# Optimization experiments

Hardware: AMD Instinct MI355X
Metric: run time of the kernel (lower is better)

## Reference

```python
import jax, jax.numpy as jnp
import numpy as np

L, H, C, V, B, T, Q = 6, 8, 512, 32000, 2, 4096, 256
N = C // H
LN_EPS = 1e-5
GN_EPS = 1e-5 * 64  # matches nn.GroupNorm(n_head, C, eps=1e-05*64)


def _shift(x):
    # ZeroPad2d((0,0,1,-1)): x[t] -> x[t-1], zero at t=0
    return jnp.concatenate([jnp.zeros_like(x[:, :1]), x[:, :-1]], axis=1)


def _layernorm(x, w):
    mu = x.mean(-1, keepdims=True)
    var = jnp.var(x, axis=-1, keepdims=True)
    return (x - mu) * jax.lax.rsqrt(var + LN_EPS) * w


def _time_mix(x, maa_k, maa_v, maa_r, maa_g, tdecay, tfaaaa, Wr, Wk, Wv, Wg, Wo, gn_w, gn_b):
    Bsz, Tlen, Cd = x.shape
    xx = _shift(x) - x
    xk = x + xx * maa_k
    xv = x + xx * maa_v
    xr = x + xx * maa_r
    xg = x + xx * maa_g
    r = (xr @ Wr.T).reshape(Bsz, Tlen, H, N).transpose(0, 2, 1, 3)   # B H T N
    k = (xk @ Wk.T).reshape(Bsz, Tlen, H, N).transpose(0, 2, 3, 1)   # B H N T
    v = (xv @ Wv.T).reshape(Bsz, Tlen, H, N).transpose(0, 2, 1, 3)   # B H T N
    g = jax.nn.silu(xg @ Wg.T)
    wdec = jnp.exp(-jnp.exp(tdecay))            # [H], per-head decay in (0,1)
    u = tfaaaa                                  # [H], 'first token' bonus
    ws = (wdec ** Q)[None, :, None, None]       # state decay across a chunk
    jj = jnp.arange(Q)
    wkv = (wdec[:, None] ** (Q - 1 - jj))[None, :, None, :]  # [1,H,1,Q]
    wb = (wdec[:, None] ** jj)[None, :, :, None]              # [1,H,Q,1]
    d = jj[:, None] - jj[None, :]                              # i - j
    # intra-chunk decay matrix: W[i,j] = u (i==j), wdec^(i-j-1) (i>j), 0 (i<j)
    Wmat = jnp.where(d > 0, wdec[:, None, None] ** jnp.maximum(d - 1, 0), 0.0)
    Wmat = (Wmat + u[:, None, None] * jnp.eye(Q, dtype=x.dtype))[None]  # [1,H,Q,Q]
    nc = Tlen // Q
    rc = r.reshape(Bsz, H, nc, Q, N).transpose(2, 0, 1, 3, 4)  # [nc,B,H,Q,N]
    kc = k.reshape(Bsz, H, N, nc, Q).transpose(3, 0, 1, 2, 4)  # [nc,B,H,N,Q]
    vc = v.reshape(Bsz, H, nc, Q, N).transpose(2, 0, 1, 3, 4)  # [nc,B,H,Q,N]

    def step(state, inp):
        rr, kk, vv = inp
        y = ((rr @ kk) * Wmat) @ vv + (rr @ state) * wb
        new_state = ws * state + (kk * wkv) @ vv
        return new_state, y

    state0 = jnp.zeros((Bsz, H, N, N), dtype=x.dtype)
    _, yc = jax.lax.scan(step, state0, (rc, kc, vc))
    y = yc.transpose(1, 2, 0, 3, 4).reshape(Bsz, H, Tlen, N).transpose(0, 2, 1, 3)  # B T H N
    # GroupNorm(n_head groups) == per (b,t,h) normalization over head dim N
    mu = y.mean(-1, keepdims=True)
    var = jnp.var(y, axis=-1, keepdims=True)
    y = (y - mu) * jax.lax.rsqrt(var + GN_EPS)
    y = y.reshape(Bsz, Tlen, Cd) * gn_w + gn_b
    return (y * g) @ Wo.T


def _channel_mix(x, cmaa_k, cmaa_r, Wck, Wcv, Wcr):
    xx = _shift(x) - x
    xk = x + xx * cmaa_k
    xr = x + xx * cmaa_r
    h = jnp.square(jax.nn.relu(xk @ Wck.T))
    h = h @ Wcv.T
    return jax.nn.sigmoid(xr @ Wcr.T) * h


def _forward(idx, wte, wpe, ln1_w, ln2_w, lnf_w, maa_k, maa_v, maa_r, maa_g, tdecay, tfaaaa,
             Wr, Wk, Wv, Wg, Wo, gn_w, gn_b, cmaa_k, cmaa_r, Wck, Wcv, Wcr):
    t = idx.shape[1]
    x = wte[idx] + wpe[:t]
    for l in range(L):
        x = x + _time_mix(_layernorm(x, ln1_w[l]), maa_k[l], maa_v[l], maa_r[l], maa_g[l],
                          tdecay[l], tfaaaa[l], Wr[l], Wk[l], Wv[l], Wg[l], Wo[l], gn_w[l], gn_b[l])
        x = x + _channel_mix(_layernorm(x, ln2_w[l]), cmaa_k[l], cmaa_r[l], Wck[l], Wcv[l], Wcr[l])
    x = _layernorm(x, lnf_w)
    logits = x[:, -1:, :] @ wte.T  # targets=None path: only last position
    return logits


def setup_inputs() -> dict:
    key = jax.random.key(0)
    ks = jax.random.split(key, 12)
    idx = jax.random.randint(ks[0], (B, T), 0, V)
    # structured per-layer init tensors (exact formulas from __init__)
    ddd = np.arange(C, dtype=np.float32) / C
    hh = np.arange(H, dtype=np.float32) / (H - 1)
    maa_k = np.zeros((L, C), np.float32); maa_v = np.zeros((L, C), np.float32)
    maa_r = np.zeros((L, C), np.float32); maa_g = np.zeros((L, C), np.float32)
    tdecay = np.zeros((L, H), np.float32); tfaaaa = np.zeros((L, H), np.float32)
    cmaa_k = np.zeros((L, C), np.float32); cmaa_r = np.zeros((L, C), np.float32)
    for l in range(L):
        r0 = l / max(L - 1, 1)
        r1 = 1.0 - l / L
        maa_k[l] = 1.0 - ddd ** r1
        maa_v[l] = 1.0 - (ddd ** r1 + 0.3 * r0)
        maa_r[l] = 1.0 - ddd ** (0.5 * r1)
        maa_g[l] = 1.0 - ddd ** (0.5 * r1)
        tdecay[l] = -6.0 + 5.0 * hh ** (0.7 + 1.3 * r0)
        tfaaaa[l] = r0 * (1.0 - hh)
        cmaa_k[l] = 1.0 - ddd ** r1
        cmaa_r[l] = 1.0 - ddd ** r1
    s = 0.02
    return {
        'idx': idx,
        'wte': jax.random.normal(ks[1], (V, C), jnp.float32) * s,
        'wpe': jax.random.normal(ks[2], (T, C), jnp.float32) * s,
        'ln1_w': jnp.ones((L, C), jnp.float32),
        'ln2_w': jnp.ones((L, C), jnp.float32),
        'lnf_w': jnp.ones((C,), jnp.float32),
        'maa_k': jnp.asarray(maa_k), 'maa_v': jnp.asarray(maa_v),
        'maa_r': jnp.asarray(maa_r), 'maa_g': jnp.asarray(maa_g),
        'tdecay': jnp.asarray(tdecay), 'tfaaaa': jnp.asarray(tfaaaa),
        'Wr': jax.random.normal(ks[3], (L, C, C), jnp.float32) * s,
        'Wk': jax.random.normal(ks[4], (L, C, C), jnp.float32) * s,
        'Wv': jax.random.normal(ks[5], (L, C, C), jnp.float32) * s,
        'Wg': jax.random.normal(ks[6], (L, C, C), jnp.float32) * s,
        'Wo': jax.random.normal(ks[7], (L, C, C), jnp.float32) * (s / np.sqrt(2 * L)),
        'gn_w': jnp.ones((L, C), jnp.float32),
        'gn_b': jnp.zeros((L, C), jnp.float32),
        'cmaa_k': jnp.asarray(cmaa_k), 'cmaa_r': jnp.asarray(cmaa_r),
        'Wck': jax.random.normal(ks[8], (L, 3 * C, C), jnp.float32) * s,
        'Wcv': jax.random.normal(ks[9], (L, C, 3 * C), jnp.float32) * s,
        'Wcr': jax.random.normal(ks[10], (L, C, C), jnp.float32) * s,
    }


def reference(idx, wte, wpe, ln1_w, ln2_w, lnf_w, maa_k, maa_v, maa_r, maa_g, tdecay, tfaaaa,
              Wr, Wk, Wv, Wg, Wo, gn_w, gn_b, cmaa_k, cmaa_r, Wck, Wcv, Wcr):
    return _forward(idx, wte, wpe, ln1_w, ln2_w, lnf_w, maa_k, maa_v, maa_r, maa_g, tdecay,
                    tfaaaa, Wr, Wk, Wv, Wg, Wo, gn_w, gn_b, cmaa_k, cmaa_r, Wck, Wcv, Wcr)
```

## Files before the change

kernel.cpp:

```cpp
#include <hip/hip_runtime.h>

#define L_ 6
#define H_ 8
#define C_ 512
#define V_ 32000
#define B_ 2
#define T_ 4096
#define Q_ 256
#define N_ 64
#define NC_ 16
#define M_ 8192

typedef unsigned short u16;
typedef __attribute__((ext_vector_type(8))) short bf16x8;
typedef __attribute__((ext_vector_type(4))) float f32x4;

__device__ __forceinline__ float bf2f(u16 u){
  return __uint_as_float(((unsigned int)u) << 16);
}
__device__ __forceinline__ u16 f2bf(float f){
  unsigned int x = __float_as_uint(f);
  return (u16)((x + 0x7fffu + ((x >> 16) & 1u)) >> 16);
}

__device__ __forceinline__ void gl_lds16(const u16* g, u16* l){
  __builtin_amdgcn_global_load_lds((const __attribute__((address_space(1))) void*)g,
                                   (__attribute__((address_space(3))) void*)l, 16, 0, 0);
}

__global__ __launch_bounds__(256) void detect_kernel(const void* __restrict__ probe,
                                                     int* __restrict__ flag){
  __shared__ int cnt;
  if (threadIdx.x == 0) cnt = 0;
  __syncthreads();
  const u16* p = (const u16*)probe;
  int c = 0;
  for (int i = threadIdx.x; i < 2048; i += 256){
    int e = (p[i] >> 7) & 0xFF;
    if (e >= 128) c++;
  }
  atomicAdd(&cnt, c);
  __syncthreads();
  if (threadIdx.x == 0) *flag = (cnt > 32) ? 1 : 0;
}

struct CvtTab { const void* s[23]; int off8[24]; };

__global__ __launch_bounds__(256) void convert_all(CvtTab t, u16* __restrict__ pool,
                                                   const int* __restrict__ flag){
  const bool f32 = (*flag != 0);
  const int total = t.off8[23];
  uint4* dp = (uint4*)pool;
  const int stride = gridDim.x * 256;
  for (int j = blockIdx.x*256 + threadIdx.x; j < total; j += stride){
    int i = 0;
    #pragma unroll
    for (int k = 1; k < 23; k++) if (j >= t.off8[k]) i = k;
    const int loc = j - t.off8[i];
    uint4 r;
    if (f32){
      const float4* sf = (const float4*)t.s[i];
      float4 a = sf[2*loc], b = sf[2*loc+1];
      r.x = (unsigned)f2bf(a.x) | ((unsigned)f2bf(a.y) << 16);
      r.y = (unsigned)f2bf(a.z) | ((unsigned)f2bf(a.w) << 16);
      r.z = (unsigned)f2bf(b.x) | ((unsigned)f2bf(b.y) << 16);
      r.w = (unsigned)f2bf(b.z) | ((unsigned)f2bf(b.w) << 16);
    } else {
      r = ((const uint4*)t.s[i])[loc];
    }
    dp[j] = r;
  }
}

__global__ __launch_bounds__(256) void embed_kernel(const int* __restrict__ idx,
    const u16* __restrict__ wte, const u16* __restrict__ wpe, float* __restrict__ x){
  int row = blockIdx.x;
  int t = row & (T_-1);
  int tok = idx[row];
  const u16* we = wte + (size_t)tok * C_;
  const u16* wp = wpe + (size_t)t * C_;
  float* xo = x + (size_t)row * C_;
  int c = threadIdx.x;
  xo[c]     = bf2f(we[c])     + bf2f(wp[c]);
  xo[c+256] = bf2f(we[c+256]) + bf2f(wp[c+256]);
}

__global__ __launch_bounds__(256) void ln_tmix_kernel(const float* __restrict__ x,
    const u16* __restrict__ w,
    const u16* __restrict__ mk, const u16* __restrict__ mv,
    const u16* __restrict__ mr, const u16* __restrict__ mg,
    u16* __restrict__ xk, u16* __restrict__ xv, u16* __restrict__ xr, u16* __restrict__ xg){
  int row = blockIdx.x; int t = row & (T_-1);
  size_t off = (size_t)row*C_;
  const float* cur = x + off;
  int c = threadIdx.x;
  float v0 = cur[c], v1 = cur[c+256];
  float p0 = 0.f, p1 = 0.f;
  if (t){ p0 = cur[c - C_]; p1 = cur[c+256 - C_]; }
  float s = v0+v1, ss = v0*v0+v1*v1;
  float sp = p0+p1, ssp = p0*p0+p1*p1;
  int lane = c & 63, wid = c >> 6;
  #pragma unroll
  for (int o=32;o>0;o>>=1){
    s  += __shfl_down(s,o,64);  ss  += __shfl_down(ss,o,64);
    sp += __shfl_down(sp,o,64); ssp += __shfl_down(ssp,o,64);
  }
  __shared__ float r1[4], r2[4], r3[4], r4[4];
  if (lane==0){ r1[wid]=s; r2[wid]=ss; r3[wid]=sp; r4[wid]=ssp; }
  __syncthreads();
  if (c==0){
    float a =r1[0]+r1[1]+r1[2]+r1[3], bq=r2[0]+r2[1]+r2[2]+r2[3];
    float ap=r3[0]+r3[1]+r3[2]+r3[3], bp=r4[0]+r4[1]+r4[2]+r4[3];
    float mu  = a *(1.f/C_); float var  = bq*(1.f/C_) - mu*mu;
    float mup = ap*(1.f/C_); float varp = bp*(1.f/C_) - mup*mup;
    r1[0]=mu;  r2[0]=rsqrtf(fmaxf(var ,0.f)+1e-5f);
    r3[0]=mup; r4[0]=rsqrtf(fmaxf(varp,0.f)+1e-5f);
  }
  __syncthreads();
  float mu=r1[0], inv=r2[0], mup=r3[0], invp=r4[0];
  #pragma unroll
  for (int p=0;p<2;p++){
    int cc = c + p*256;
    float wc = bf2f(w[cc]);
    float xc = ((p?v1:v0)-mu)*inv*wc;
    float xp = t ? ((p?p1:p0)-mup)*invp*wc : 0.f;
    float xx = xp - xc;
    xk[off+cc] = f2bf(xc + xx*bf2f(mk[cc]));
    xv[off+cc] = f2bf(xc + xx*bf2f(mv[cc]));
    xr[off+cc] = f2bf(xc + xx*bf2f(mr[cc]));
    xg[off+cc] = f2bf(xc + xx*bf2f(mg[cc]));
  }
}

__global__ __launch_bounds__(256) void ln_cmix_kernel(const float* __restrict__ x,
    const u16* __restrict__ w,
    const u16* __restrict__ mk, const u16* __restrict__ mr,
    u16* __restrict__ xk, u16* __restrict__ xr){
  int row = blockIdx.x; int t = row & (T_-1);
  size_t off = (size_t)row*C_;
  const float* cur = x + off;
  int c = threadIdx.x;
  float v0 = cur[c], v1 = cur[c+256];
  float p0 = 0.f, p1 = 0.f;
  if (t){ p0 = cur[c - C_]; p1 = cur[c+256 - C_]; }
  float s = v0+v1, ss = v0*v0+v1*v1;
  float sp = p0+p1, ssp = p0*p0+p1*p1;
  int lane = c & 63, wid = c >> 6;
  #pragma unroll
  for (int o=32;o>0;o>>=1){
    s  += __shfl_down(s,o,64);  ss  += __shfl_down(ss,o,64);
    sp += __shfl_down(sp,o,64); ssp += __shfl_down(ssp,o,64);
  }
  __shared__ float r1[4], r2[4], r3[4], r4[4];
  if (lane==0){ r1[wid]=s; r2[wid]=ss; r3[wid]=sp; r4[wid]=ssp; }
  __syncthreads();
  if (c==0){
    float a =r1[0]+r1[1]+r1[2]+r1[3], bq=r2[0]+r2[1]+r2[2]+r2[3];
    float ap=r3[0]+r3[1]+r3[2]+r3[3], bp=r4[0]+r4[1]+r4[2]+r4[3];
    float mu  = a *(1.f/C_); float var  = bq*(1.f/C_) - mu*mu;
    float mup = ap*(1.f/C_); float varp = bp*(1.f/C_) - mup*mup;
    r1[0]=mu;  r2[0]=rsqrtf(fmaxf(var ,0.f)+1e-5f);
    r3[0]=mup; r4[0]=rsqrtf(fmaxf(varp,0.f)+1e-5f);
  }
  __syncthreads();
  float mu=r1[0], inv=r2[0], mup=r3[0], invp=r4[0];
  #pragma unroll
  for (int p=0;p<2;p++){
    int cc = c + p*256;
    float wc = bf2f(w[cc]);
    float xc = ((p?v1:v0)-mu)*inv*wc;
    float xp = t ? ((p?p1:p0)-mup)*invp*wc : 0.f;
    float xx = xp - xc;
    xk[off+cc] = f2bf(xc + xx*bf2f(mk[cc]));
    xr[off+cc] = f2bf(xc + xx*bf2f(mr[cc]));
  }
}

__global__ __launch_bounds__(256) void lnf_last(const float* __restrict__ x,
    const u16* __restrict__ w, float* __restrict__ xf){
  int b = blockIdx.x;
  const float* xr = x + ((size_t)b*T_ + (T_-1))*C_;
  int c = threadIdx.x;
  float v0 = xr[c], v1 = xr[c+256];
  float s = v0+v1, ss = v0*v0+v1*v1;
  int lane = c & 63, wid = c >> 6;
  #pragma unroll
  for (int o=32;o>0;o>>=1){ s += __shfl_down(s,o,64); ss += __shfl_down(ss,o,64); }
  __shared__ float r1[4], r2[4];
  if (lane==0){ r1[wid]=s; r2[wid]=ss; }
  __syncthreads();
  if (c==0){
    float a=r1[0]+r1[1]+r1[2]+r1[3], bq=r2[0]+r2[1]+r2[2]+r2[3];
    float mu = a*(1.f/C_);
    float var = bq*(1.f/C_) - mu*mu;
    r1[0]=mu; r2[0]=rsqrtf(fmaxf(var,0.f)+1e-5f);
  }
  __syncthreads();
  float mu=r1[0], inv=r2[0];
  xf[b*C_+c]     = (v0-mu)*inv*bf2f(w[c]);
  xf[b*C_+c+256] = (v1-mu)*inv*bf2f(w[c+256]);
}

#define ACT_F32 0
#define ACT_RELU2_BF16 1
#define ACT_ADD_F32 2
#define ACT_BF16 3
#define ACT_CMIX 4
#define ACT_KT 5
#define ACT_VT 6

template<int ACT>
__device__ __forceinline__ void gemm_mfma_body(const u16* __restrict__ X, const u16* __restrict__ W,
    float* __restrict__ Yf, u16* __restrict__ Yb, const float* __restrict__ Aux,
    u16* __restrict__ Yt, const u16* __restrict__ td,
    int Ndim, int Kdim, int bm, int bn){
  __shared__ __align__(16) u16 Al[128*64];
  __shared__ __align__(16) u16 Bl[64*64];
  const int tid = threadIdx.x;
  const int wv = tid >> 6, ln = tid & 63;
  const int m16 = ln & 15, q = ln >> 4;

  f32x4 acc[2][4];
  #pragma unroll
  for (int i=0;i<2;i++)
    #pragma unroll
    for (int j=0;j<4;j++) acc[i][j] = f32x4{0.f,0.f,0.f,0.f};

  const int r0 = wv*8 + (ln >> 3);
  const int c0 = (ln & 7)*8;
  const u16* ga = X + (size_t)(bm + r0)*Kdim + c0;
  const u16* gb = W + (size_t)(bn + r0)*Kdim + c0;
  u16* la = Al + r0*64 + c0;
  u16* lb = Bl + r0*64 + c0;

  for (int k0=0; k0<Kdim; k0+=64){
    #pragma unroll
    for (int s=0;s<4;s++)
      gl_lds16(ga + (size_t)(s*32)*Kdim + k0, la + s*2048);
    #pragma unroll
    for (int s=0;s<2;s++)
      gl_lds16(gb + (size_t)(s*32)*Kdim + k0, lb + s*2048);
    __syncthreads();
    #pragma unroll
    for (int kh=0; kh<2; kh++){
      bf16x8 af[2], bfr[4];
      #pragma unroll
      for (int i=0;i<2;i++) af[i]  = *(const bf16x8*)(Al + (wv*32 + i*16 + m16)*64 + kh*32 + q*8);
      #pragma unroll
      for (int j=0;j<4;j++) bfr[j] = *(const bf16x8*)(Bl + (j*16 + m16)*64 + kh*32 + q*8);
      #pragma unroll
      for (int i=0;i<2;i++)
        #pragma unroll
        for (int j=0;j<4;j++)
          acc[i][j] = __builtin_amdgcn_mfma_f32_16x16x32_bf16(af[i], bfr[j], acc[i][j], 0, 0, 0);
    }
    __syncthreads();
  }

  if (ACT==ACT_KT || ACT==ACT_VT){
    float wdec_s = 0.f;
    if (ACT==ACT_KT) wdec_s = expf(-expf(bf2f(td[bn>>6])));
    #pragma unroll
    for (int i=0;i<2;i++){
      int row = bm + wv*32 + i*16 + q*4;
      int bb = row >> 12;
      int tt = row & (T_-1);
      int tloc = row & (Q_-1);
      float wsc[4];
      if (ACT==ACT_KT){
        #pragma unroll
        for (int r=0;r<4;r++) wsc[r] = powf(wdec_s, (float)(Q_-1-tloc-r));
      }
      #pragma unroll
      for (int j=0;j<4;j++){
        int col = bn + j*16 + m16;
        int hh = col >> 6, n = col & 63;
        union { ushort4 v; u16 e[4]; } pk;
        #pragma unroll
        for (int r=0;r<4;r++){
          float v = acc[i][j][r];
          if (ACT==ACT_KT){
            Yb[(size_t)(row+r)*Ndim + col] = f2bf(v);
            pk.e[r] = f2bf(v * wsc[r]);
          } else {
            pk.e[r] = f2bf(v);
          }
        }
        *(ushort4*)(Yt + ((size_t)((bb*8+hh)*64 + n))*T_ + tt) = pk.v;
      }
    }
    return;
  }
  #pragma unroll
  for (int i=0;i<2;i++){
    int row = bm + wv*32 + i*16 + q*4;
    #pragma unroll
    for (int j=0;j<4;j++){
      int col = bn + j*16 + m16;
      #pragma unroll
      for (int r=0;r<4;r++){
        size_t off = (size_t)(row + r)*Ndim + col;
        float v = acc[i][j][r];
        if (ACT==ACT_F32) Yf[off] = v;
        else if (ACT==ACT_RELU2_BF16){ float rr = v>0.f ? v : 0.f; Yb[off] = f2bf(rr*rr); }
        else if (ACT==ACT_BF16) Yb[off] = f2bf(v);
        else if (ACT==ACT_CMIX){ float rr = Aux[off]; Yf[off] += v/(1.f+expf(-rr)); }
        else Yf[off] += v;
      }
    }
  }
}

template<int ACT>
__global__ __launch_bounds__(256,4) void gemm_mfma(const u16* __restrict__ X, const u16* __restrict__ W,
    float* __restrict__ Yf, u16* __restrict__ Yb, int Ndim, int Kdim){
  gemm_mfma_body<ACT>(X, W, Yf, Yb, nullptr, nullptr, nullptr, Ndim, Kdim,
                      blockIdx.x*128, blockIdx.y*64);
}

__global__ __launch_bounds__(256,4) void gemm4_mfma(const u16* __restrict__ Abase,
    const u16* __restrict__ W0, const u16* __restrict__ W1,
    const u16* __restrict__ W2, const u16* __restrict__ W3,
    u16* __restrict__ Rb, u16* __restrict__ Kb, u16* __restrict__ Kt,
    u16* __restrict__ Vt, u16* __restrict__ Gb, const u16* __restrict__ td){
  const size_t MC = (size_t)M_*C_;
  const int bm = blockIdx.x*128, bn = blockIdx.y*64;
  switch (blockIdx.z){
    case 0:  gemm_mfma_body<ACT_BF16>(Abase + 2*MC, W0, nullptr, Rb, nullptr, nullptr, nullptr,
                                      C_, C_, bm, bn); break;
    case 1:  gemm_mfma_body<ACT_KT>(Abase, W1, nullptr, Kb, nullptr, Kt, td,
                                    C_, C_, bm, bn); break;
    case 2:  gemm_mfma_body<ACT_VT>(Abase + 1*MC, W2, nullptr, nullptr, nullptr, Vt, nullptr,
                                    C_, C_, bm, bn); break;
    default: gemm_mfma_body<ACT_BF16>(Abase + 3*MC, W3, nullptr, Gb, nullptr, nullptr, nullptr,
                                      C_, C_, bm, bn); break;
  }
}

__global__ __launch_bounds__(256,4) void gemm_ck_cr(const u16* __restrict__ MK, const u16* __restrict__ Wck,
    u16* __restrict__ H1, const u16* __restrict__ MV, const u16* __restrict__ Wcr,
    float* __restrict__ RR){
  if (blockIdx.y < 24)
    gemm_mfma_body<ACT_RELU2_BF16>(MK, Wck, nullptr, H1, nullptr, nullptr, nullptr, 3*C_, C_,
                                   blockIdx.x*128, blockIdx.y*64);
  else
    gemm_mfma_body<ACT_F32>(MV, Wcr, RR, nullptr, nullptr, nullptr, nullptr, C_, C_,
                            blockIdx.x*128, (blockIdx.y-24)*64);
}

__global__ __launch_bounds__(256,4) void gemm_cmix(const u16* __restrict__ H1, const u16* __restrict__ Wcv,
    float* __restrict__ X, const float* __restrict__ RR){
  gemm_mfma_body<ACT_CMIX>(H1, Wcv, X, nullptr, RR, nullptr, nullptr, C_, 3*C_,
                           blockIdx.x*128, blockIdx.y*64);
}

__global__ __launch_bounds__(256) void wkv_intra_mfma(const u16* __restrict__ Rb,
    const u16* __restrict__ Kb, const u16* __restrict__ Vt,
    const u16* __restrict__ td, const u16* __restrict__ tf, float* __restrict__ y){
  __shared__ float wpow[Q_];
  __shared__ __align__(16) u16 P[4][16][72];
  const int c = blockIdx.x >> 2, ip = blockIdx.x & 3;
  const int bh = blockIdx.y, b = bh >> 3, h = bh & 7;
  const int tid = threadIdx.x, wv = tid >> 6, ln = tid & 63;
  const int m16 = ln & 15, q = ln >> 4;
  const float wdec = expf(-expf(bf2f(td[h])));
  const float uu = bf2f(tf[h]);
  wpow[tid] = powf(wdec, (float)tid);
  __syncthreads();
  const size_t base = ((size_t)b*T_ + (size_t)c*Q_)*C_ + h*N_;
  const int iw0 = ip*64 + wv*16;
  const u16* rrow = Rb + base + (size_t)(iw0 + m16)*C_;
  bf16x8 af0 = *(const bf16x8*)(rrow + q*8);
  bf16x8 af1 = *(const bf16x8*)(rrow + 32 + q*8);
  f32x4 acc[4];
  #pragma unroll
  for (int nt=0;nt<4;++nt) acc[nt] = f32x4{0.f,0.f,0.f,0.f};
  const int irow = iw0 + q*4;
  const u16* vtb = Vt + (size_t)(bh*N_)*T_ + (size_t)c*Q_;
  for (int jt=0; jt<=ip; ++jt){
    f32x4 s[4];
    #pragma unroll
    for (int j2=0;j2<4;++j2) s[j2] = f32x4{0.f,0.f,0.f,0.f};
    #pragma unroll
    for (int j2=0;j2<4;++j2){
      const u16* kr = Kb + base + (size_t)(jt*64 + j2*16 + m16)*C_;
      bf16x8 b0 = *(const bf16x8*)(kr + q*8);
      bf16x8 b1 = *(const bf16x8*)(kr + 32 + q*8);
      s[j2] = __builtin_amdgcn_mfma_f32_16x16x32_bf16(af0, b0, s[j2], 0,0,0);
      s[j2] = __builtin_amdgcn_mfma_f32_16x16x32_bf16(af1, b1, s[j2], 0,0,0);
    }
    #pragma unroll
    for (int j2=0;j2<4;++j2){
      int jc = jt*64 + j2*16 + m16;
      #pragma unroll
      for (int r=0;r<4;++r){
        int ic = irow + r;
        float w = (jc < ic) ? wpow[ic-jc-1] : ((jc==ic) ? uu : 0.f);
        P[wv][q*4+r][j2*16+m16] = f2bf(s[j2][r]*w);
      }
    }
    __asm__ volatile("s_waitcnt lgkmcnt(0)" ::: "memory");
    #pragma unroll
    for (int kp=0;kp<2;++kp){
      bf16x8 ap = *(const bf16x8*)&P[wv][m16][kp*32 + q*8];
      #pragma unroll
      for (int nt=0;nt<4;++nt){
        bf16x8 bv = *(const bf16x8*)(vtb + (size_t)(nt*16 + m16)*T_ + jt*64 + kp*32 + q*8);
        acc[nt] = __builtin_amdgcn_mfma_f32_16x16x32_bf16(ap, bv, acc[nt], 0,0,0);
      }
    }
  }
  #pragma unroll
  for (int nt=0;nt<4;++nt)
    #pragma unroll
    for (int r=0;r<4;++r)
      y[base + (size_t)(irow + r)*C_ + nt*16 + m16] = acc[nt][r];
}

__global__ __launch_bounds__(256) void wkv_state_mfma(const u16* __restrict__ Kt,
    const u16* __restrict__ Vt, float* __restrict__ S){
  const int c = blockIdx.x, bh = blockIdx.y;
  const int tid = threadIdx.x, wv = tid >> 6, ln = tid & 63;
  const int m16 = ln & 15, q = ln >> 4;
  const u16* ka = Kt + (size_t)(bh*N_ + wv*16 + m16)*T_ + c*Q_;
  const u16* vb = Vt + (size_t)(bh*N_ + m16)*T_ + c*Q_;
  f32x4 acc[4];
  #pragma unroll
  for (int nt=0;nt<4;++nt) acc[nt] = f32x4{0.f,0.f,0.f,0.f};
  #pragma unroll
  for (int ks=0; ks<8; ++ks){
    bf16x8 af = *(const bf16x8*)(ka + ks*32 + q*8);
    #pragma unroll
    for (int nt=0;nt<4;++nt){
      bf16x8 bv = *(const bf16x8*)(vb + (size_t)(nt*16)*T_ + ks*32 + q*8);
      acc[nt] = __builtin_amdgcn_mfma_f32_16x16x32_bf16(af, bv, acc[nt], 0,0,0);
    }
  }
  float* Sp = S + ((size_t)bh*NC_ + c)*(N_*N_);
  #pragma unroll
  for (int nt=0;nt<4;++nt)
    #pragma unroll
    for (int r=0;r<4;++r)
      Sp[(wv*16 + q*4 + r)*N_ + nt*16 + m16] = acc[nt][r];
}

__global__ __launch_bounds__(256) void wkv_prefix(float* __restrict__ S, const u16* __restrict__ td){
  const int bh = blockIdx.x, h = bh&7;
  const float wdec = expf(-expf(bf2f(td[h])));
  const float wsd = powf(wdec, (float)Q_);
  float* Sp = S + (size_t)bh*NC_*N_*N_;
  for (int e=threadIdx.x; e<N_*N_; e+=256){
    float cur = 0.f;
    for (int cc=0;cc<NC_;++cc){
      float sc = Sp[(size_t)cc*N_*N_ + e];
      Sp[(size_t)cc*N_*N_ + e] = cur;
      cur = wsd*cur + sc;
    }
  }
}

__global__ __launch_bounds__(256) void wkv_inter_gn(const u16* __restrict__ Rb, const float* __restrict__ S,
    const u16* __restrict__ td, const float* __restrict__ y,
    const u16* __restrict__ gnw, const u16* __restrict__ gnb, const u16* __restrict__ g,
    u16* __restrict__ out){
  __shared__ float st[64][65];
  __shared__ float rs[64][68];
  __shared__ float wpow[Q_];
  const int c = blockIdx.x>>2, ip = blockIdx.x&3;
  const int bh = blockIdx.y, b = bh>>3, h = bh&7;
  const int tid = threadIdx.x, tx = tid&15, ty = tid>>4;
  const float wdec = expf(-expf(bf2f(td[h])));
  wpow[tid] = powf(wdec, (float)tid);
  const float* Sp = S + ((size_t)bh*NC_ + c)*(N_*N_);
  for (int e=tid;e<N_*N_;e+=256) st[e>>6][e&63] = Sp[e];
  const size_t base = ((size_t)b*T_ + (size_t)c*Q_)*C_ + h*N_;
  const int i0 = ip*64;
  {
    const int rr = tid >> 6, cc2 = tid & 63;
    for (int it=0;it<16;++it){ int i=it*4+rr; rs[i][cc2]=bf2f(Rb[base+(size_t)(i0+i)*C_+cc2]); }
  }
  __syncthreads();
  float acc[4][4] = {};
  for (int kk=0;kk<N_;++kk){
    float rv[4], sv[4];
    #pragma unroll
    for (int ii=0;ii<4;ii++) rv[ii]=rs[ty*4+ii][kk];
    #pragma unroll
    for (int nn=0;nn<4;nn++) sv[nn]=st[kk][tx*4+nn];
    #pragma unroll
    for (int ii=0;ii<4;ii++)
      #pragma unroll
      for (int nn=0;nn<4;nn++) acc[ii][nn]+=rv[ii]*sv[nn];
  }
  #pragma unroll
  for (int ii=0;ii<4;ii++){
    int il = i0+ty*4+ii;
    size_t roff = base + (size_t)il*C_;
    float w = wpow[il];
    float4 yv = *(const float4*)(y + roff + tx*4);
    float val[4] = {yv.x, yv.y, yv.z, yv.w};
    float s=0.f, ss=0.f;
    #pragma unroll
    for (int nn=0;nn<4;nn++){
      float v = val[nn] + w*acc[ii][nn];
      val[nn]=v; s+=v; ss+=v*v;
    }
    #pragma unroll
    for (int o=8;o>0;o>>=1){ s+=__shfl_xor(s,o,64); ss+=__shfl_xor(ss,o,64); }
    float mu = s*(1.f/N_);
    float var = ss*(1.f/N_) - mu*mu;
    float inv = rsqrtf(fmaxf(var,0.f) + 6.4e-4f);
    union { ushort4 v; u16 e[4]; } gv, ov;
    gv.v = *(const ushort4*)(g + roff + tx*4);
    #pragma unroll
    for (int nn=0;nn<4;nn++){
      int ci = h*N_ + tx*4 + nn;
      float gg = bf2f(gv.e[nn]);
      float sil = gg/(1.f+expf(-gg));
      ov.e[nn] = f2bf(((val[nn]-mu)*inv*bf2f(gnw[ci]) + bf2f(gnb[ci]))*sil);
    }
    *(ushort4*)(out + roff + tx*4) = ov.v;
  }
}

__global__ __launch_bounds__(256) void logits_kernel(const float* __restrict__ xf,
    const u16* __restrict__ wte, void* __restrict__ out, const int* __restrict__ flag){
  const int wid = threadIdx.x>>6, lane = threadIdx.x&63;
  const int gw = blockIdx.x*4 + wid;
  const int b = gw / V_, v = gw - b*V_;
  const u16* wrow = wte + (size_t)v*C_;
  const float* xr = xf + b*C_;
  union {uint4 q; u16 h[8];} uu;
  uu.q = *(const uint4*)(wrow + lane*8);
  float s = 0.f;
  #pragma unroll
  for (int j=0;j<8;j++) s += bf2f(uu.h[j])*xr[lane*8+j];
  #pragma unroll
  for (int o=32;o>0;o>>=1) s += __shfl_down(s,o,64);
  if (lane==0){
    size_t o = (size_t)b*V_ + v;
    if (*flag) ((float*)out)[o] = s;
    else       ((u16*)out)[o]   = f2bf(s);
  }
}

extern "C" void kernel_launch(void* const* d_in, const int* in_sizes, int n_in,
                              void* d_out, int out_size, void* d_ws, size_t ws_size,
                              hipStream_t stream){
  (void)out_size; (void)ws_size; (void)n_in;
  const int* idx  = (const int*)d_in[0];

  char* ws = (char*)d_ws;
  const size_t MC  = (size_t)M_*C_;
  size_t o = 0;
  int* flag = (int*)(ws + o);            o += 1024;
  float* X   = (float*)(ws + o);         o += MC*4;
  float* Y   = (float*)(ws + o);         o += MC*4;
  u16* MK = (u16*)(ws + o);              o += MC*2;
  u16* MV = (u16*)(ws + o);              o += MC*2;
  u16* MR = (u16*)(ws + o);              o += MC*2;
  u16* MG = (u16*)(ws + o);              o += MC*2;
  u16* Rb = (u16*)(ws + o);              o += MC*2;
  u16* Kb = (u16*)(ws + o);              o += MC*2;
  u16* Kt = (u16*)(ws + o);              o += MC*2;
  u16* Gb = (u16*)(ws + o);              o += MC*2;
  u16* Vt = (u16*)(ws + o);              o += MC*2;
  float* XF = (float*)(ws + o);          o += 65536;
  u16* pool = (u16*)(ws + o);
  u16* YGN = MK;
  float* S  = (float*)MR;
  u16* H1 = Rb;
  float* RR = (float*)MR;

  detect_kernel<<<1,256,0,stream>>>(d_in[12], flag);
  u16* cw[24];
  CvtTab tab;
  {
    size_t poff = 0;
    int acc8 = 0;
    tab.off8[0] = 0;
    for (int i=1;i<24;i++){
      cw[i] = pool + poff; poff += (size_t)in_sizes[i];
      tab.s[i-1] = d_in[i];
      acc8 += in_sizes[i] >> 3;
      tab.off8[i] = acc8;
    }
  }
  convert_all<<<2048,256,0,stream>>>(tab, pool, flag);
  const u16* wte  = cw[1];  const u16* wpe  = cw[2];
  const u16* ln1w = cw[3];  const u16* ln2w = cw[4];  const u16* lnfw = cw[5];
  const u16* maak = cw[6];  const u16* maav = cw[7];
  const u16* maar = cw[8];  const u16* maag = cw[9];
  const u16* tdec = cw[10]; const u16* tfir = cw[11];
  const u16* Wr   = cw[12]; const u16* Wk   = cw[13]; const u16* Wv   = cw[14];
  const u16* Wg   = cw[15]; const u16* Wo   = cw[16];
  const u16* gnw  = cw[17]; const u16* gnb  = cw[18];
  const u16* cmk  = cw[19]; const u16* cmr  = cw[20];
  const u16* Wck  = cw[21]; const u16* Wcv  = cw[22]; const u16* Wcr  = cw[23];

  embed_kernel<<<M_,256,0,stream>>>(idx,wte,wpe,X);
  dim3 gsq(M_/128, C_/64);
  dim3 g4 (M_/128, C_/64, 4);
  dim3 gckcr(M_/128, 32);
  for (int l=0;l<L_;++l){
    ln_tmix_kernel<<<M_,256,0,stream>>>(X, ln1w+l*C_, maak+l*C_, maav+l*C_, maar+l*C_,
                                        maag+l*C_, MK,MV,MR,MG);
    gemm4_mfma<<<g4,256,0,stream>>>(MK, Wr+(size_t)l*C_*C_, Wk+(size_t)l*C_*C_,
                                    Wv+(size_t)l*C_*C_, Wg+(size_t)l*C_*C_,
                                    Rb, Kb, Kt, Vt, Gb, tdec+l*H_);
    wkv_intra_mfma<<<dim3(NC_*4, B_*H_),256,0,stream>>>(Rb,Kb,Vt, tdec+l*H_, tfir+l*H_, Y);
    wkv_state_mfma<<<dim3(NC_, B_*H_),256,0,stream>>>(Kt, Vt, S);
    wkv_prefix<<<B_*H_,256,0,stream>>>(S, tdec+l*H_);
    wkv_inter_gn<<<dim3(NC_*4, B_*H_),256,0,stream>>>(Rb, S, tdec+l*H_, Y,
                                                      gnw+l*C_, gnb+l*C_, Gb, YGN);
    gemm_mfma<ACT_ADD_F32><<<gsq,256,0,stream>>>(YGN, Wo+(size_t)l*C_*C_, X, nullptr, C_, C_);
    ln_cmix_kernel<<<M_,256,0,stream>>>(X, ln2w+l*C_, cmk+l*C_, cmr+l*C_, MK, MV);
    gemm_ck_cr<<<gckcr,256,0,stream>>>(MK, Wck+(size_t)l*3*C_*C_, H1,
                                       MV, Wcr+(size_t)l*C_*C_, RR);
    gemm_cmix<<<gsq,256,0,stream>>>(H1, Wcv+(size_t)l*C_*3*C_, X, RR);
  }
  lnf_last<<<B_,256,0,stream>>>(X, lnfw, XF);
  logits_kernel<<<(B_*V_)/4,256,0,stream>>>(XF, wte, d_out, flag);
}
```

Measured before the change: 1.667 ms.

## Fuse WKV intra/inter kernels, stage transposed K/V stores, bf16 sigmoid gate, per-tensor convert

Merges the intra-chunk WKV kernel into the inter-chunk GroupNorm kernel so the fp32 Y intermediate lives in LDS instead of round-tripping through global memory. The K/V transposed outputs are first staged in shared memory and written with coalesced 16-byte stores. The channel-mix receptance sigmoid is now computed in the Wcr GEMM epilogue and stored as bf16, which halves that buffer and moves the exp out of the cmix GEMM. The convert kernel assigns blocks per tensor and unrolls its loops. Risks: precision loss from the bf16 gate, higher LDS use in the fused kernel lowering occupancy, and a changed Wcv layer offset (3*C_*C_ vs C_*3*C_, which is numerically equal).

Result: no change. 1.673 ms (+0.4%).

```diff
diff --git a/kernel.cpp b/kernel.cpp
--- a/kernel.cpp
+++ b/kernel.cpp
@@ -44,31 +44,55 @@
   if (threadIdx.x == 0) *flag = (cnt > 32) ? 1 : 0;
 }
 
-struct CvtTab { const void* s[23]; int off8[24]; };
+struct CvtTab { const void* s[23]; int off8[24]; int bstart[24]; };
 
 __global__ __launch_bounds__(256) void convert_all(CvtTab t, u16* __restrict__ pool,
                                                    const int* __restrict__ flag){
-  const bool f32 = (*flag != 0);
-  const int total = t.off8[23];
-  uint4* dp = (uint4*)pool;
-  const int stride = gridDim.x * 256;
-  for (int j = blockIdx.x*256 + threadIdx.x; j < total; j += stride){
-    int i = 0;
-    #pragma unroll
-    for (int k = 1; k < 23; k++) if (j >= t.off8[k]) i = k;
-    const int loc = j - t.off8[i];
-    uint4 r;
-    if (f32){
-      const float4* sf = (const float4*)t.s[i];
-      float4 a = sf[2*loc], b = sf[2*loc+1];
-      r.x = (unsigned)f2bf(a.x) | ((unsigned)f2bf(a.y) << 16);
-      r.y = (unsigned)f2bf(a.z) | ((unsigned)f2bf(a.w) << 16);
-      r.z = (unsigned)f2bf(b.x) | ((unsigned)f2bf(b.y) << 16);
-      r.w = (unsigned)f2bf(b.z) | ((unsigned)f2bf(b.w) << 16);
-    } else {
-      r = ((const uint4*)t.s[i])[loc];
-    }
-    dp[j] = r;
+  int i = 0;
+  #pragma unroll
+  for (int k = 1; k < 23; k++) if ((int)blockIdx.x >= t.bstart[k]) i = k;
+  const void* sp = t.s[0];
+  #pragma unroll
+  for (int k = 1; k < 23; k++) if (i == k) sp = t.s[k];
+  const int n8 = t.off8[i+1] - t.off8[i];
+  const int nb = t.bstart[i+1] - t.bstart[i];
+  const int lb = (int)blockIdx.x - t.bstart[i];
+  uint4* dp = (uint4*)pool + t.off8[i];
+  const int stride = nb * 256;
+  int j = lb*256 + (int)threadIdx.x;
+  if (*flag){
+    const float4* sf = (const float4*)sp;
+    for (; j + stride < n8; j += 2*stride){
+      float4 a0 = sf[2*j], a1 = sf[2*j+1];
+      int j2 = j + stride;
+      float4 b0 = sf[2*j2], b1 = sf[2*j2+1];
+      uint4 r0, r1;
+      r0.x = (unsigned)f2bf(a0.x) | ((unsigned)f2bf(a0.y) << 16);
+      r0.y = (unsigned)f2bf(a0.z) | ((unsigned)f2bf(a0.w) << 16);
+      r0.z = (unsigned)f2bf(a1.x) | ((unsigned)f2bf(a1.y) << 16);
+      r0.w = (unsigned)f2bf(a1.z) | ((unsigned)f2bf(a1.w) << 16);
+      r1.x = (unsigned)f2bf(b0.x) | ((unsigned)f2bf(b0.y) << 16);
+      r1.y = (unsigned)f2bf(b0.z) | ((unsigned)f2bf(b0.w) << 16);
+      r1.z = (unsigned)f2bf(b1.x) | ((unsigned)f2bf(b1.y) << 16);
+      r1.w = (unsigned)f2bf(b1.z) | ((unsigned)f2bf(b1.w) << 16);
+      dp[j] = r0; dp[j2] = r1;
+    }
+    for (; j < n8; j += stride){
+      float4 a0 = sf[2*j], a1 = sf[2*j+1];
+      uint4 r0;
+      r0.x = (unsigned)f2bf(a0.x) | ((unsigned)f2bf(a0.y) << 16);
+      r0.y = (unsigned)f2bf(a0.z) | ((unsigned)f2bf(a0.w) << 16);
+      r0.z = (unsigned)f2bf(a1.x) | ((unsigned)f2bf(a1.y) << 16);
+      r0.w = (unsigned)f2bf(a1.z) | ((unsigned)f2bf(a1.w) << 16);
+      dp[j] = r0;
+    }
+  } else {
+    const uint4* s4 = (const uint4*)sp;
+    for (; j + 3*stride < n8; j += 4*stride){
+      uint4 a = s4[j], b = s4[j+stride], c = s4[j+2*stride], d = s4[j+3*stride];
+      dp[j] = a; dp[j+stride] = b; dp[j+2*stride] = c; dp[j+3*stride] = d;
+    }
+    for (; j < n8; j += stride) dp[j] = s4[j];
   }
 }
 
@@ -208,14 +232,16 @@
 #define ACT_CMIX 4
 #define ACT_KT 5
 #define ACT_VT 6
+#define ACT_SIG_BF16 7
 
 template<int ACT>
 __device__ __forceinline__ void gemm_mfma_body(const u16* __restrict__ X, const u16* __restrict__ W,
-    float* __restrict__ Yf, u16* __restrict__ Yb, const float* __restrict__ Aux,
+    float* __restrict__ Yf, u16* __restrict__ Yb, const u16* __restrict__ AuxB,
     u16* __restrict__ Yt, const u16* __restrict__ td,
     int Ndim, int Kdim, int bm, int bn){
-  __shared__ __align__(16) u16 Al[128*64];
-  __shared__ __align__(16) u16 Bl[64*64];
+  __shared__ __align__(16) u16 SH[128*64 + 64*64];
+  u16* Al = SH;
+  u16* Bl = SH + 128*64;
   const int tid = threadIdx.x;
   const int wv = tid >> 6, ln = tid & 63;
   const int m16 = ln & 15, q = ln >> 4;
@@ -258,37 +284,38 @@
   }
 
   if (ACT==ACT_KT || ACT==ACT_VT){
-    float wdec_s = 0.f;
-    if (ACT==ACT_KT) wdec_s = expf(-expf(bf2f(td[bn>>6])));
+    u16* TT = SH;
+    const float wdec_s = (ACT==ACT_KT) ? expf(-expf(bf2f(td[(bn>>6)&7]))) : 0.f;
+    const int tchunk0 = bm & (Q_-1);
     #pragma unroll
     for (int i=0;i<2;i++){
-      int row = bm + wv*32 + i*16 + q*4;
-      int bb = row >> 12;
-      int tt = row & (T_-1);
-      int tloc = row & (Q_-1);
-      float wsc[4];
-      if (ACT==ACT_KT){
-        #pragma unroll
-        for (int r=0;r<4;r++) wsc[r] = powf(wdec_s, (float)(Q_-1-tloc-r));
-      }
+      const int tloc = wv*32 + i*16 + q*4;
       #pragma unroll
       for (int j=0;j<4;j++){
-        int col = bn + j*16 + m16;
-        int hh = col >> 6, n = col & 63;
+        const int n = j*16 + m16;
         union { ushort4 v; u16 e[4]; } pk;
         #pragma unroll
         for (int r=0;r<4;r++){
           float v = acc[i][j][r];
           if (ACT==ACT_KT){
-            Yb[(size_t)(row+r)*Ndim + col] = f2bf(v);
-            pk.e[r] = f2bf(v * wsc[r]);
+            Yb[(size_t)(bm + tloc + r)*Ndim + (bn + n)] = f2bf(v);
+            pk.e[r] = f2bf(v * powf(wdec_s, (float)(Q_-1 - (tchunk0 + tloc + r))));
           } else {
             pk.e[r] = f2bf(v);
           }
         }
-        *(ushort4*)(Yt + ((size_t)((bb*8+hh)*64 + n))*T_ + tt) = pk.v;
+        *(ushort4*)&TT[n*136 + tloc] = pk.v;
       }
     }
+    __syncthreads();
+    const int bb = bm >> 12, tt0 = bm & (T_-1);
+    const int hh = (bn >> 6) & 7;
+    const int nn2 = wv*16 + (ln>>2), seg = ln & 3;
+    const u16* srcp = TT + nn2*136 + seg*32;
+    u16* dstp = Yt + ((size_t)(((bb<<3)+hh)*64 + nn2))*T_ + tt0 + seg*32;
+    #pragma unroll
+    for (int k2=0;k2<4;k2++)
+      *(uint4*)(dstp + k2*8) = *(const uint4*)(srcp + k2*8);
     return;
   }
   #pragma unroll
@@ -304,7 +331,8 @@
         if (ACT==ACT_F32) Yf[off] = v;
         else if (ACT==ACT_RELU2_BF16){ float rr = v>0.f ? v : 0.f; Yb[off] = f2bf(rr*rr); }
         else if (ACT==ACT_BF16) Yb[off] = f2bf(v);
-        else if (ACT==ACT_CMIX){ float rr = Aux[off]; Yf[off] += v/(1.f+expf(-rr)); }
+        else if (ACT==ACT_SIG_BF16) Yb[off] = f2bf(1.f/(1.f+expf(-v)));
+        else if (ACT==ACT_CMIX){ Yf[off] += v * bf2f(AuxB[off]); }
         else Yf[off] += v;
       }
     }
@@ -339,82 +367,19 @@
 
 __global__ __launch_bounds__(256,4) void gemm_ck_cr(const u16* __restrict__ MK, const u16* __restrict__ Wck,
     u16* __restrict__ H1, const u16* __restrict__ MV, const u16* __restrict__ Wcr,
-    float* __restrict__ RR){
+    u16* __restrict__ RRb){
   if (blockIdx.y < 24)
     gemm_mfma_body<ACT_RELU2_BF16>(MK, Wck, nullptr, H1, nullptr, nullptr, nullptr, 3*C_, C_,
                                    blockIdx.x*128, blockIdx.y*64);
   else
-    gemm_mfma_body<ACT_F32>(MV, Wcr, RR, nullptr, nullptr, nullptr, nullptr, C_, C_,
-                            blockIdx.x*128, (blockIdx.y-24)*64);
+    gemm_mfma_body<ACT_SIG_BF16>(MV, Wcr, nullptr, RRb, nullptr, nullptr, nullptr, C_, C_,
+                                 blockIdx.x*128, (blockIdx.y-24)*64);
 }
 
 __global__ __launch_bounds__(256,4) void gemm_cmix(const u16* __restrict__ H1, const u16* __restrict__ Wcv,
-    float* __restrict__ X, const float* __restrict__ RR){
-  gemm_mfma_body<ACT_CMIX>(H1, Wcv, X, nullptr, RR, nullptr, nullptr, C_, 3*C_,
+    float* __restrict__ X, const u16* __restrict__ RRb){
+  gemm_mfma_body<ACT_CMIX>(H1, Wcv, X, nullptr, RRb, nullptr, nullptr, C_, 3*C_,
                            blockIdx.x*128, blockIdx.y*64);
-}
-
-__global__ __launch_bounds__(256) void wkv_intra_mfma(const u16* __restrict__ Rb,
-    const u16* __restrict__ Kb, const u16* __restrict__ Vt,
-    const u16* __restrict__ td, const u16* __restrict__ tf, float* __restrict__ y){
-  __shared__ float wpow[Q_];
-  __shared__ __align__(16) u16 P[4][16][72];
-  const int c = blockIdx.x >> 2, ip = blockIdx.x & 3;
-  const int bh = blockIdx.y, b = bh >> 3, h = bh & 7;
-  const int tid = threadIdx.x, wv = tid >> 6, ln = tid & 63;
-  const int m16 = ln & 15, q = ln >> 4;
-  const float wdec = expf(-expf(bf2f(td[h])));
-  const float uu = bf2f(tf[h]);
-  wpow[tid] = powf(wdec, (float)tid);
-  __syncthreads();
-  const size_t base = ((size_t)b*T_ + (size_t)c*Q_)*C_ + h*N_;
-  const int iw0 = ip*64 + wv*16;
-  const u16* rrow = Rb + base + (size_t)(iw0 + m16)*C_;
-  bf16x8 af0 = *(const bf16x8*)(rrow + q*8);
-  bf16x8 af1 = *(const bf16x8*)(rrow + 32 + q*8);
-  f32x4 acc[4];
-  #pragma unroll
-  for (int nt=0;nt<4;++nt) acc[nt] = f32x4{0.f,0.f,0.f,0.f};
-  const int irow = iw0 + q*4;
-  const u16* vtb = Vt + (size_t)(bh*N_)*T_ + (size_t)c*Q_;
-  for (int jt=0; jt<=ip; ++jt){
-    f32x4 s[4];
-    #pragma unroll
-    for (int j2=0;j2<4;++j2) s[j2] = f32x4{0.f,0.f,0.f,0.f};
-    #pragma unroll
-    for (int j2=0;j2<4;++j2){
-      const u16* kr = Kb + base + (size_t)(jt*64 + j2*16 + m16)*C_;
-      bf16x8 b0 = *(const bf16x8*)(kr + q*8);
-      bf16x8 b1 = *(const bf16x8*)(kr + 32 + q*8);
-      s[j2] = __builtin_amdgcn_mfma_f32_16x16x32_bf16(af0, b0, s[j2], 0,0,0);
-      s[j2] = __builtin_amdgcn_mfma_f32_16x16x32_bf16(af1, b1, s[j2], 0,0,0);
-    }
-    #pragma unroll
-    for (int j2=0;j2<4;++j2){
-      int jc = jt*64 + j2*16 + m16;
-      #pragma unroll
-      for (int r=0;r<4;++r){
-        int ic = irow + r;
-        float w = (jc < ic) ? wpow[ic-jc-1] : ((jc==ic) ? uu : 0.f);
-        P[wv][q*4+r][j2*16+m16] = f2bf(s[j2][r]*w);
-      }
-    }
-    __asm__ volatile("s_waitcnt lgkmcnt(0)" ::: "memory");
-    #pragma unroll
-    for (int kp=0;kp<2;++kp){
-      bf16x8 ap = *(const bf16x8*)&P[wv][m16][kp*32 + q*8];
-      #pragma unroll
-      for (int nt=0;nt<4;++nt){
-        bf16x8 bv = *(const bf16x8*)(vtb + (size_t)(nt*16 + m16)*T_ + jt*64 + kp*32 + q*8);
-        acc[nt] = __builtin_amdgcn_mfma_f32_16x16x32_bf16(ap, bv, acc[nt], 0,0,0);
-      }
-    }
-  }
-  #pragma unroll
-  for (int nt=0;nt<4;++nt)
-    #pragma unroll
-    for (int r=0;r<4;++r)
-      y[base + (size_t)(irow + r)*C_ + nt*16 + m16] = acc[nt][r];
 }
 
 __global__ __launch_bounds__(256) void wkv_state_mfma(const u16* __restrict__ Kt,
@@ -459,50 +424,110 @@
   }
 }
 
-__global__ __launch_bounds__(256) void wkv_inter_gn(const u16* __restrict__ Rb, const float* __restrict__ S,
-    const u16* __restrict__ td, const float* __restrict__ y,
+__global__ __launch_bounds__(256) void wkv_fused(const u16* __restrict__ Rb,
+    const u16* __restrict__ Kb, const u16* __restrict__ Vt, const float* __restrict__ S,
+    const u16* __restrict__ td, const u16* __restrict__ tf,
     const u16* __restrict__ gnw, const u16* __restrict__ gnb, const u16* __restrict__ g,
     u16* __restrict__ out){
-  __shared__ float st[64][65];
+  __shared__ float wpow[Q_];
+  __shared__ float st[64][68];
   __shared__ float rs[64][68];
-  __shared__ float wpow[Q_];
+  __shared__ __align__(16) float ylds[64][68];
+  u16 (*P)[16][72] = reinterpret_cast<u16(*)[16][72]>(&ylds[0][0]);
   const int c = blockIdx.x>>2, ip = blockIdx.x&3;
   const int bh = blockIdx.y, b = bh>>3, h = bh&7;
-  const int tid = threadIdx.x, tx = tid&15, ty = tid>>4;
+  const int tid = threadIdx.x, wv = tid >> 6, ln = tid & 63;
+  const int m16 = ln & 15, q = ln >> 4;
+  const int tx = tid&15, ty = tid>>4;
   const float wdec = expf(-expf(bf2f(td[h])));
+  const float uu = bf2f(tf[h]);
   wpow[tid] = powf(wdec, (float)tid);
   const float* Sp = S + ((size_t)bh*NC_ + c)*(N_*N_);
   for (int e=tid;e<N_*N_;e+=256) st[e>>6][e&63] = Sp[e];
   const size_t base = ((size_t)b*T_ + (size_t)c*Q_)*C_ + h*N_;
   const int i0 = ip*64;
   {
-    const int rr = tid >> 6, cc2 = tid & 63;
-    for (int it=0;it<16;++it){ int i=it*4+rr; rs[i][cc2]=bf2f(Rb[base+(size_t)(i0+i)*C_+cc2]); }
-  }
-  __syncthreads();
-  float acc[4][4] = {};
-  for (int kk=0;kk<N_;++kk){
-    float rv[4], sv[4];
-    #pragma unroll
-    for (int ii=0;ii<4;ii++) rv[ii]=rs[ty*4+ii][kk];
-    #pragma unroll
-    for (int nn=0;nn<4;nn++) sv[nn]=st[kk][tx*4+nn];
-    #pragma unroll
-    for (int ii=0;ii<4;ii++)
-      #pragma unroll
-      for (int nn=0;nn<4;nn++) acc[ii][nn]+=rv[ii]*sv[nn];
+    const int rrr = tid >> 6, cc2 = tid & 63;
+    for (int it=0;it<16;++it){ int i=it*4+rrr; rs[i][cc2]=bf2f(Rb[base+(size_t)(i0+i)*C_+cc2]); }
+  }
+  __syncthreads();
+  const int iw0 = ip*64 + wv*16;
+  const u16* rrow = Rb + base + (size_t)(iw0 + m16)*C_;
+  bf16x8 af0 = *(const bf16x8*)(rrow + q*8);
+  bf16x8 af1 = *(const bf16x8*)(rrow + 32 + q*8);
+  f32x4 acc[4];
+  #pragma unroll
+  for (int nt=0;nt<4;++nt) acc[nt] = f32x4{0.f,0.f,0.f,0.f};
+  const int irow = iw0 + q*4;
+  const u16* vtb = Vt + (size_t)(bh*N_)*T_ + (size_t)c*Q_;
+  for (int jt=0; jt<=ip; ++jt){
+    f32x4 s[4];
+    #pragma unroll
+    for (int j2=0;j2<4;++j2) s[j2] = f32x4{0.f,0.f,0.f,0.f};
+    #pragma unroll
+    for (int j2=0;j2<4;++j2){
+      const u16* kr = Kb + base + (size_t)(jt*64 + j2*16 + m16)*C_;
+      bf16x8 b0 = *(const bf16x8*)(kr + q*8);
+      bf16x8 b1 = *(const bf16x8*)(kr + 32 + q*8);
+      s[j2] = __builtin_amdgcn_mfma_f32_16x16x32_bf16(af0, b0, s[j2], 0,0,0);
+      s[j2] = __builtin_amdgcn_mfma_f32_16x16x32_bf16(af1, b1, s[j2], 0,0,0);
+    }
+    #pragma unroll
+    for (int j2=0;j2<4;++j2){
+      int jc = jt*64 + j2*16 + m16;
+      #pragma unroll
+      for (int r=0;r<4;++r){
+        int ic = irow + r;
+        float w = (jc < ic) ? wpow[ic-jc-1] : ((jc==ic) ? uu : 0.f);
+        P[wv][q*4+r][j2*16+m16] = f2bf(s[j2][r]*w);
+      }
+    }
+    __asm__ volatile("s_waitcnt lgkmcnt(0)" ::: "memory");
+    #pragma unroll
+    for (int kp=0;kp<2;++kp){
+      bf16x8 ap = *(const bf16x8*)&P[wv][m16][kp*32 + q*8];
+      #pragma unroll
+      for (int nt=0;nt<4;++nt){
+        bf16x8 bv = *(const bf16x8*)(vtb + (size_t)(nt*16 + m16)*T_ + jt*64 + kp*32 + q*8);
+        acc[nt] = __builtin_amdgcn_mfma_f32_16x16x32_bf16(ap, bv, acc[nt], 0,0,0);
+      }
+    }
+  }
+  __syncthreads();
+  #pragma unroll
+  for (int nt=0;nt<4;++nt)
+    #pragma unroll
+    for (int r=0;r<4;++r)
+      ylds[wv*16 + q*4 + r][nt*16 + m16] = acc[nt][r];
+  __syncthreads();
+  float acc2[4][4] = {};
+  #pragma unroll
+  for (int kk4=0;kk4<16;++kk4){
+    f32x4 sv[4], rv[4];
+    #pragma unroll
+    for (int kkk=0;kkk<4;++kkk) sv[kkk] = *(const f32x4*)&st[kk4*4+kkk][tx*4];
+    #pragma unroll
+    for (int ii=0;ii<4;++ii)    rv[ii]  = *(const f32x4*)&rs[ty*4+ii][kk4*4];
+    #pragma unroll
+    for (int ii=0;ii<4;++ii)
+      #pragma unroll
+      for (int kkk=0;kkk<4;++kkk)
+        #pragma unroll
+        for (int nn=0;nn<4;++nn)
+          acc2[ii][nn] += rv[ii][kkk]*sv[kkk][nn];
   }
   #pragma unroll
   for (int ii=0;ii<4;ii++){
-    int il = i0+ty*4+ii;
+    int tl = ty*4+ii;
+    int il = i0 + tl;
     size_t roff = base + (size_t)il*C_;
     float w = wpow[il];
-    float4 yv = *(const float4*)(y + roff + tx*4);
-    float val[4] = {yv.x, yv.y, yv.z, yv.w};
+    f32x4 yv = *(const f32x4*)&ylds[tl][tx*4];
+    float val[4];
     float s=0.f, ss=0.f;
     #pragma unroll
     for (int nn=0;nn<4;nn++){
-      float v = val[nn] + w*acc[ii][nn];
+      float v = yv[nn] + w*acc2[ii][nn];
       val[nn]=v; s+=v; ss+=v*v;
     }
     #pragma unroll
@@ -555,7 +580,6 @@
   size_t o = 0;
   int* flag = (int*)(ws + o);            o += 1024;
   float* X   = (float*)(ws + o);         o += MC*4;
-  float* Y   = (float*)(ws + o);         o += MC*4;
   u16* MK = (u16*)(ws + o);              o += MC*2;
   u16* MV = (u16*)(ws + o);              o += MC*2;
   u16* MR = (u16*)(ws + o);              o += MC*2;
@@ -570,23 +594,30 @@
   u16* YGN = MK;
   float* S  = (float*)MR;
   u16* H1 = Rb;
-  float* RR = (float*)MR;
+  u16* RRb = MR;
 
   detect_kernel<<<1,256,0,stream>>>(d_in[12], flag);
   u16* cw[24];
   CvtTab tab;
+  int nblocks;
   {
-    size_t poff = 0;
-    int acc8 = 0;
-    tab.off8[0] = 0;
+    size_t poff = 0; int acc8 = 0, bacc = 0;
+    long long total8 = 0;
+    for (int i=1;i<24;i++) total8 += (long long)(in_sizes[i] >> 3);
     for (int i=1;i<24;i++){
       cw[i] = pool + poff; poff += (size_t)in_sizes[i];
       tab.s[i-1] = d_in[i];
-      acc8 += in_sizes[i] >> 3;
-      tab.off8[i] = acc8;
-    }
-  }
-  convert_all<<<2048,256,0,stream>>>(tab, pool, flag);
+      tab.off8[i-1] = acc8;
+      tab.bstart[i-1] = bacc;
+      int n8 = in_sizes[i] >> 3;
+      int nb = (int)(((long long)n8 * 2048 + total8 - 1) / total8);
+      if (nb < 1) nb = 1;
+      acc8 += n8; bacc += nb;
+    }
+    tab.off8[23] = acc8; tab.bstart[23] = bacc;
+    nblocks = bacc;
+  }
+  convert_all<<<nblocks,256,0,stream>>>(tab, pool, flag);
   const u16* wte  = cw[1];  const u16* wpe  = cw[2];
   const u16* ln1w = cw[3];  const u16* ln2w = cw[4];  const u16* lnfw = cw[5];
   const u16* maak = cw[6];  const u16* maav = cw[7];
@@ -608,16 +639,15 @@
     gemm4_mfma<<<g4,256,0,stream>>>(MK, Wr+(size_t)l*C_*C_, Wk+(size_t)l*C_*C_,
                                     Wv+(size_t)l*C_*C_, Wg+(size_t)l*C_*C_,
                                     Rb, Kb, Kt, Vt, Gb, tdec+l*H_);
-    wkv_intra_mfma<<<dim3(NC_*4, B_*H_),256,0,stream>>>(Rb,Kb,Vt, tdec+l*H_, tfir+l*H_, Y);
     wkv_state_mfma<<<dim3(NC_, B_*H_),256,0,stream>>>(Kt, Vt, S);
     wkv_prefix<<<B_*H_,256,0,stream>>>(S, tdec+l*H_);
-    wkv_inter_gn<<<dim3(NC_*4, B_*H_),256,0,stream>>>(Rb, S, tdec+l*H_, Y,
-                                                      gnw+l*C_, gnb+l*C_, Gb, YGN);
+    wkv_fused<<<dim3(NC_*4, B_*H_),256,0,stream>>>(Rb, Kb, Vt, S, tdec+l*H_, tfir+l*H_,
+                                                   gnw+l*C_, gnb+l*C_, Gb, YGN);
     gemm_mfma<ACT_ADD_F32><<<gsq,256,0,stream>>>(YGN, Wo+(size_t)l*C_*C_, X, nullptr, C_, C_);
     ln_cmix_kernel<<<M_,256,0,stream>>>(X, ln2w+l*C_, cmk+l*C_, cmr+l*C_, MK, MV);
     gemm_ck_cr<<<gckcr,256,0,stream>>>(MK, Wck+(size_t)l*3*C_*C_, H1,
-                                       MV, Wcr+(size_t)l*C_*C_, RR);
-    gemm_cmix<<<gsq,256,0,stream>>>(H1, Wcv+(size_t)l*C_*3*C_, X, RR);
+                                       MV, Wcr+(size_t)l*C_*C_, RRb);
+    gemm_cmix<<<gsq,256,0,stream>>>(H1, Wcv+(size_t)l*3*C_*C_, X, RRb);
   }
   lnf_last<<<B_,256,0,stream>>>(X, lnfw, XF);
   logits_kernel<<<(B_*V_)/4,256,0,stream>>>(XF, wte, d_out, flag);
```
